# Kernel optimization log

Measured on AMD Instinct MI355X. Metric: run time of the kernel, lower is better.

## Reference

```python
import jax, jax.numpy as jnp
import numpy as np

B, D = 8, 256
N_LIVE, K_NEW = 10000, 32
KC = N_LIVE + K_NEW
N_SAMPLES = 100
EPSILON = 0.1


def setup_inputs() -> dict:
    key = jax.random.key(0)
    k1, k2, k3, k4, k5, k6 = jax.random.split(key, 6)
    return {
        "xt": jax.random.normal(k1, (B, D), dtype=jnp.float32),
        "live_x0": jax.random.normal(k2, (B, N_LIVE, D), dtype=jnp.float32),
        "live_ll": jax.random.normal(k3, (B, N_LIVE, 1), dtype=jnp.float32),
        "x0": jax.random.normal(k4, (B, K_NEW, D), dtype=jnp.float32),
        "ll": jax.random.normal(k5, (B, K_NEW, 1), dtype=jnp.float32),
        "t_scale": jnp.float32(0.5),
        "boot_idx": jax.random.randint(k6, (N_SAMPLES, B, KC), 0, KC, dtype=jnp.int32),
    }


def reference(xt, live_x0, live_ll, x0, ll, t_scale, boot_idx):
    # --- spotlight_score core math ---
    # gaussian correction for the new particles: 0.5*||x0-xt||^2/sigma^2 + log(sigma)
    diff_new = x0 - xt[:, None, :]                                   # [B,K,D]
    corr_new = 0.5 * jnp.sum(diff_new ** 2, axis=-1, keepdims=True) / t_scale ** 2  # [B,K,1]
    current_x0 = jnp.concatenate([live_x0, x0], axis=1)              # [B,Kc,D]
    current_ll = jnp.concatenate(
        [live_ll, ll + corr_new + jnp.log(t_scale)], axis=1)         # [B,Kc,1]

    diff = current_x0 - xt[:, None, :]                               # [B,Kc,D]
    use_ll = (current_ll
              - 0.5 * jnp.sum(diff ** 2, axis=-1, keepdims=True) / t_scale ** 2
              - jnp.log(t_scale))                                    # [B,Kc,1]

    scores_p = diff / t_scale                                        # [B,Kc,D] per-particle scores
    logits = use_ll[..., 0]                                          # [B,Kc]

    # --- check_convergence: bootstrap resampled softmax reductions ---
    def body(carry, idx_n):                                          # idx_n: [B,Kc]
        s = jnp.take_along_axis(scores_p, idx_n[:, :, None], axis=1)  # [B,Kc,D]
        l = jnp.take_along_axis(logits, idx_n, axis=1)                # [B,Kc]
        w = jax.nn.softmax(l, axis=1)
        return carry, jnp.einsum('bk,bkd->bd', w, s)                  # [B,D]

    _, boot = jax.lax.scan(body, None, boot_idx)                      # [N,B,D]
    sigma_v = jnp.std(boot, axis=0, ddof=1)                           # [B,D] (torch.std is unbiased)
    converged = jnp.all(sigma_v < EPSILON * t_scale, axis=1)          # [B]

    # --- final importance-weighted score ---
    w = jax.nn.softmax(logits, axis=1)                                # [B,Kc]
    score = jnp.einsum('bk,bkd->bd', w, scores_p)                     # [B,D]
    return score, converged
```

## Files before the change

### kernel.cpp

```cpp
#include <hip/hip_runtime.h>
#include <math.h>

#define B 8
#define D 256
#define N_LIVE 10000
#define K_NEW 32
#define KC 10032
#define NS 100
#define NROW 101
#define EPS 0.1f
#define CAP 1024
#define ACT_CUT 87.0f
#define LBLK 627
#define BMAX_STRIDE 640

#define WS_HDR    0
#define WS_BMAX   160
#define WS_LOGITS (WS_BMAX + B * BMAX_STRIDE)
#define WS_ACTE   (WS_LOGITS + B * KC)
#define WS_ACTI   (WS_ACTE + B * CAP)
#define WS_LUT    (WS_ACTI + B * CAP)
#define WS_BOOT   (WS_LUT + B * KC / 2)

__global__ __launch_bounds__(256) void k_logits(
    const float* __restrict__ xt, const float* __restrict__ live_x0,
    const float* __restrict__ live_ll, const float* __restrict__ x0n,
    const float* __restrict__ lln, const float* __restrict__ ts_p,
    float* __restrict__ logits, float* __restrict__ bmax) {
  int b = blockIdx.y;
  int w = threadIdx.x >> 6;
  int lane = threadIdx.x & 63;
  int k0 = blockIdx.x * 16 + w * 4;
  float4 c = ((const float4*)(xt + b * D))[lane];

  float s[4];
#pragma unroll
  for (int p = 0; p < 4; p++) {
    int k = k0 + p;
    const float* src = (k < N_LIVE)
        ? (live_x0 + ((size_t)b * N_LIVE + k) * D)
        : (x0n + ((size_t)b * K_NEW + (k - N_LIVE)) * D);
    float4 v = ((const float4*)src)[lane];
    float dx = v.x - c.x, dy = v.y - c.y, dz = v.z - c.z, dw = v.w - c.w;
    s[p] = dx * dx + dy * dy + dz * dz + dw * dw;
  }
#pragma unroll
  for (int off = 32; off; off >>= 1) {
    s[0] += __shfl_xor(s[0], off);
    s[1] += __shfl_xor(s[1], off);
    s[2] += __shfl_xor(s[2], off);
    s[3] += __shfl_xor(s[3], off);
  }
  __shared__ float wlog[4];
  if (lane == 0) {
    float ts = *ts_p;
    float inv2 = 0.5f / (ts * ts), lts = logf(ts);
    float4 o;
    float* ov = &o.x;
#pragma unroll
    for (int p = 0; p < 4; p++) {
      int k = k0 + p;
      ov[p] = (k < N_LIVE)
          ? live_ll[(size_t)b * N_LIVE + k] - s[p] * inv2 - lts
          : lln[(size_t)b * K_NEW + (k - N_LIVE)];
    }
    *(float4*)(logits + (size_t)b * KC + k0) = o;
    wlog[w] = fmaxf(fmaxf(o.x, o.y), fmaxf(o.z, o.w));
  }
  __syncthreads();
  if (threadIdx.x == 0)
    bmax[b * BMAX_STRIDE + blockIdx.x] =
        fmaxf(fmaxf(wlog[0], wlog[1]), fmaxf(wlog[2], wlog[3]));
}

__global__ __launch_bounds__(256) void k_bmax(
    const float* __restrict__ bmax, float* __restrict__ hdr) {
  int b = blockIdx.x;
  int tid = threadIdx.x;
  float m = -INFINITY;
  for (int i = tid; i < LBLK; i += 256) m = fmaxf(m, bmax[b * BMAX_STRIDE + i]);
#pragma unroll
  for (int off = 32; off; off >>= 1) m = fmaxf(m, __shfl_xor(m, off));
  __shared__ float sm[4];
  if ((tid & 63) == 0) sm[tid >> 6] = m;
  __syncthreads();
  if (tid == 0)
    hdr[b * 16] = fmaxf(fmaxf(sm[0], sm[1]), fmaxf(sm[2], sm[3]));
}

__global__ __launch_bounds__(256) void k_select(
    const float* __restrict__ logits, const float* __restrict__ hdrM,
    unsigned* __restrict__ hdr, float* __restrict__ act_e,
    int* __restrict__ act_idx, unsigned short* __restrict__ lut) {
  int b = blockIdx.y;
  int tid = blockIdx.x * 256 + threadIdx.x;
  float M = hdrM[b * 16];
  const float* lg = logits + (size_t)b * KC;
  int* cnt = (int*)&hdr[128 + b];
  for (int k = tid; k < KC; k += 8 * 256) {
    float l = lg[k];
    unsigned short v = 0;
    if (l > M - ACT_CUT) {
      int pos = atomicAdd(cnt, 1);
      if (pos < CAP) {
        act_e[b * CAP + pos] = expf(l - M);
        act_idx[b * CAP + pos] = k;
        v = (unsigned short)(pos + 1);
      }
    }
    lut[(size_t)b * KC + k] = v;
  }
}

__global__ __launch_bounds__(256) void k_boot(
    const float* __restrict__ live_x0, const float* __restrict__ x0n,
    const float* __restrict__ act_e, const int* __restrict__ act_idx,
    const unsigned* __restrict__ hdr, const unsigned short* __restrict__ lut,
    const int* __restrict__ boot_idx, float* __restrict__ boot) {
  int n = blockIdx.x;
  int b = blockIdx.y;
  int tid = threadIdx.x;
  __shared__ int cnt[CAP];
  __shared__ float wval[CAP];
  __shared__ int widx[CAP];
  __shared__ int snnz;
  __shared__ float sden[4];
  int A = min((int)hdr[128 + b], CAP);
  for (int i = tid; i < A; i += 256) cnt[i] = 0;
  if (tid == 0) snnz = 0;
  __syncthreads();

  if (n < NS) {
    const int4* row = (const int4*)(boot_idx + ((size_t)n * B + b) * KC);
    const unsigned short* lutb = lut + (size_t)b * KC;
    for (int k = tid; k < KC / 4; k += 256) {
      int4 v = row[k];
      int t;
      t = lutb[v.x]; if (t) atomicAdd(&cnt[t - 1], 1);
      t = lutb[v.y]; if (t) atomicAdd(&cnt[t - 1], 1);
      t = lutb[v.z]; if (t) atomicAdd(&cnt[t - 1], 1);
      t = lutb[v.w]; if (t) atomicAdd(&cnt[t - 1], 1);
    }
  } else {
    for (int i = tid; i < A; i += 256) cnt[i] = 1;
  }
  __syncthreads();

  float dpart = 0.f;
  for (int i = tid; i < A; i += 256) {
    int c = cnt[i];
    if (c) {
      float w = (float)c * act_e[b * CAP + i];
      int pos = atomicAdd(&snnz, 1);
      wval[pos] = w;
      widx[pos] = act_idx[b * CAP + i];
      dpart += w;
    }
  }
#pragma unroll
  for (int off = 32; off; off >>= 1) dpart += __shfl_xor(dpart, off);
  if ((tid & 63) == 0) sden[tid >> 6] = dpart;
  __syncthreads();
  float inv = 1.f / (sden[0] + sden[1] + sden[2] + sden[3]);
  int nnz = snnz;

  const float* lx = live_x0 + (size_t)b * N_LIVE * D;
  const float* nx = x0n + (size_t)b * K_NEW * D;
  float acc0 = 0.f, acc1 = 0.f;
  int p = 0;
  for (; p + 1 < nnz; p += 2) {
    int j0 = widx[p], j1 = widx[p + 1];
    const float* r0 = (j0 < N_LIVE) ? (lx + (size_t)j0 * D) : (nx + (size_t)(j0 - N_LIVE) * D);
    const float* r1 = (j1 < N_LIVE) ? (lx + (size_t)j1 * D) : (nx + (size_t)(j1 - N_LIVE) * D);
    float x0v = r0[tid], x1v = r1[tid];
    acc0 = fmaf(wval[p], x0v, acc0);
    acc1 = fmaf(wval[p + 1], x1v, acc1);
  }
  if (p < nnz) {
    int j = widx[p];
    const float* xr = (j < N_LIVE) ? (lx + (size_t)j * D) : (nx + (size_t)(j - N_LIVE) * D);
    acc0 = fmaf(wval[p], xr[tid], acc0);
  }
  boot[((size_t)b * NROW + n) * D + tid] = (acc0 + acc1) * inv;
}

__global__ __launch_bounds__(256) void k_final(
    const float* __restrict__ boot, const float* __restrict__ xt,
    const float* __restrict__ ts_p, float* __restrict__ out) {
  int b = blockIdx.x;
  int d = threadIdx.x;
  float ts = *ts_p;
  const float* bb = boot + (size_t)b * NROW * D + d;
  float sum = 0.f;
#pragma unroll 4
  for (int n = 0; n < NS; n++) sum += bb[(size_t)n * D];
  float mean = sum / (float)NS;
  float vs = 0.f;
#pragma unroll 4
  for (int n = 0; n < NS; n++) { float t = bb[(size_t)n * D] - mean; vs += t * t; }
  float sigma_raw = sqrtf(vs / (float)(NS - 1));
  bool ok = (sigma_raw / ts) < (EPS * ts);
  out[(size_t)b * D + d] = (bb[(size_t)NS * D] - xt[(size_t)b * D + d]) / ts;
  unsigned long long m = __ballot(ok);
  __shared__ int wok[4];
  if ((d & 63) == 0) wok[d >> 6] = (m == 0xFFFFFFFFFFFFFFFFull) ? 1 : 0;
  __syncthreads();
  if (d == 0) out[(size_t)B * D + b] = (wok[0] & wok[1] & wok[2] & wok[3]) ? 1.0f : 0.0f;
}

extern "C" void kernel_launch(void* const* d_in, const int* in_sizes, int n_in,
                              void* d_out, int out_size, void* d_ws, size_t ws_size,
                              hipStream_t stream) {
  const float* xt       = (const float*)d_in[0];
  const float* live_x0  = (const float*)d_in[1];
  const float* live_ll  = (const float*)d_in[2];
  const float* x0n      = (const float*)d_in[3];
  const float* lln      = (const float*)d_in[4];
  const float* ts_p     = (const float*)d_in[5];
  const int*   boot_idx = (const int*)d_in[6];
  float* out = (float*)d_out;
  float* ws  = (float*)d_ws;

  float* hdrM              = ws + WS_HDR;
  unsigned* hdr            = (unsigned*)(ws + WS_HDR);
  float* bmax              = ws + WS_BMAX;
  float* logits            = ws + WS_LOGITS;
  float* act_e             = ws + WS_ACTE;
  int*   act_idx           = (int*)(ws + WS_ACTI);
  unsigned short* lut      = (unsigned short*)(ws + WS_LUT);
  float* boot              = ws + WS_BOOT;

  hipMemsetAsync(hdr, 0, 160 * sizeof(unsigned), stream);

  k_logits<<<dim3(LBLK, B), 256, 0, stream>>>(xt, live_x0, live_ll, x0n, lln, ts_p, logits, bmax);
  k_bmax<<<dim3(B), 256, 0, stream>>>(bmax, hdrM);
  k_select<<<dim3(8, B), 256, 0, stream>>>(logits, hdrM, hdr, act_e, act_idx, lut);
  k_boot<<<dim3(NROW, B), 256, 0, stream>>>(live_x0, x0n, act_e, act_idx, hdr, lut, boot_idx, boot);
  k_final<<<dim3(B), 256, 0, stream>>>(boot, xt, ts_p, out);
}
```

Before: 189.3 us.

## Split boot gather across wavefronts with float4 loads; double rows per logits block

In the bootstrap kernel, each of the four wavefronts now walks a strided quarter of the nonzero particle list and loads whole rows as float4 per lane. The four partial accumulators are then reduced through shared memory. The aim is fewer, wider memory transactions and more independent loads in flight per block, at the cost of an extra barrier and shared-memory reduction. The logits kernel also handles 8 rows per wavefront instead of 4, halving the block count, with guards added for the padded tail block.

```diff
diff --git a/kernel.cpp b/kernel.cpp
--- a/kernel.cpp
+++ b/kernel.cpp
@@ -11,8 +11,8 @@
 #define EPS 0.1f
 #define CAP 1024
 #define ACT_CUT 87.0f
-#define LBLK 627
-#define BMAX_STRIDE 640
+#define LBLK 314
+#define BMAX_STRIDE 320
 
 #define WS_HDR    0
 #define WS_BMAX   160
@@ -30,13 +30,15 @@
   int b = blockIdx.y;
   int w = threadIdx.x >> 6;
   int lane = threadIdx.x & 63;
-  int k0 = blockIdx.x * 16 + w * 4;
+  int k0 = blockIdx.x * 32 + w * 8;
+  bool valid = (k0 < KC);
+  int kb = valid ? k0 : 0;
   float4 c = ((const float4*)(xt + b * D))[lane];
 
-  float s[4];
-#pragma unroll
-  for (int p = 0; p < 4; p++) {
-    int k = k0 + p;
+  float s[8];
+#pragma unroll
+  for (int p = 0; p < 8; p++) {
+    int k = kb + p;
     const float* src = (k < N_LIVE)
         ? (live_x0 + ((size_t)b * N_LIVE + k) * D)
         : (x0n + ((size_t)b * K_NEW + (k - N_LIVE)) * D);
@@ -46,26 +48,31 @@
   }
 #pragma unroll
   for (int off = 32; off; off >>= 1) {
-    s[0] += __shfl_xor(s[0], off);
-    s[1] += __shfl_xor(s[1], off);
-    s[2] += __shfl_xor(s[2], off);
-    s[3] += __shfl_xor(s[3], off);
+#pragma unroll
+    for (int p = 0; p < 8; p++) s[p] += __shfl_xor(s[p], off);
   }
   __shared__ float wlog[4];
   if (lane == 0) {
     float ts = *ts_p;
     float inv2 = 0.5f / (ts * ts), lts = logf(ts);
-    float4 o;
-    float* ov = &o.x;
-#pragma unroll
-    for (int p = 0; p < 4; p++) {
-      int k = k0 + p;
-      ov[p] = (k < N_LIVE)
+    float o[8];
+#pragma unroll
+    for (int p = 0; p < 8; p++) {
+      int k = kb + p;
+      o[p] = (k < N_LIVE)
           ? live_ll[(size_t)b * N_LIVE + k] - s[p] * inv2 - lts
           : lln[(size_t)b * K_NEW + (k - N_LIVE)];
     }
-    *(float4*)(logits + (size_t)b * KC + k0) = o;
-    wlog[w] = fmaxf(fmaxf(o.x, o.y), fmaxf(o.z, o.w));
+    if (valid) {
+      float4 o0 = {o[0], o[1], o[2], o[3]}, o1 = {o[4], o[5], o[6], o[7]};
+      *(float4*)(logits + (size_t)b * KC + kb) = o0;
+      *(float4*)(logits + (size_t)b * KC + kb + 4) = o1;
+      float m = fmaxf(fmaxf(fmaxf(o[0], o[1]), fmaxf(o[2], o[3])),
+                      fmaxf(fmaxf(o[4], o[5]), fmaxf(o[6], o[7])));
+      wlog[w] = m;
+    } else {
+      wlog[w] = -INFINITY;
+    }
   }
   __syncthreads();
   if (threadIdx.x == 0)
@@ -120,9 +127,11 @@
   int n = blockIdx.x;
   int b = blockIdx.y;
   int tid = threadIdx.x;
+  int nw = tid >> 6, lane = tid & 63;
   __shared__ int cnt[CAP];
   __shared__ float wval[CAP];
   __shared__ int widx[CAP];
+  __shared__ float4 part[4][64];
   __shared__ int snnz;
   __shared__ float sden[4];
   int A = min((int)hdr[128 + b], CAP);
@@ -166,22 +175,42 @@
 
   const float* lx = live_x0 + (size_t)b * N_LIVE * D;
   const float* nx = x0n + (size_t)b * K_NEW * D;
-  float acc0 = 0.f, acc1 = 0.f;
-  int p = 0;
-  for (; p + 1 < nnz; p += 2) {
-    int j0 = widx[p], j1 = widx[p + 1];
-    const float* r0 = (j0 < N_LIVE) ? (lx + (size_t)j0 * D) : (nx + (size_t)(j0 - N_LIVE) * D);
-    const float* r1 = (j1 < N_LIVE) ? (lx + (size_t)j1 * D) : (nx + (size_t)(j1 - N_LIVE) * D);
-    float x0v = r0[tid], x1v = r1[tid];
-    acc0 = fmaf(wval[p], x0v, acc0);
-    acc1 = fmaf(wval[p + 1], x1v, acc1);
+  float4 a0 = {0.f, 0.f, 0.f, 0.f}, a1 = {0.f, 0.f, 0.f, 0.f};
+  int p = nw;
+  for (; p + 4 < nnz; p += 8) {
+    int j0 = widx[p], j1 = widx[p + 4];
+    float w0 = wval[p], w1 = wval[p + 4];
+    const float4* r0 = (const float4*)((j0 < N_LIVE) ? (lx + (size_t)j0 * D)
+                                                     : (nx + (size_t)(j0 - N_LIVE) * D));
+    const float4* r1 = (const float4*)((j1 < N_LIVE) ? (lx + (size_t)j1 * D)
+                                                     : (nx + (size_t)(j1 - N_LIVE) * D));
+    float4 v0 = r0[lane], v1 = r1[lane];
+    a0.x = fmaf(w0, v0.x, a0.x); a0.y = fmaf(w0, v0.y, a0.y);
+    a0.z = fmaf(w0, v0.z, a0.z); a0.w = fmaf(w0, v0.w, a0.w);
+    a1.x = fmaf(w1, v1.x, a1.x); a1.y = fmaf(w1, v1.y, a1.y);
+    a1.z = fmaf(w1, v1.z, a1.z); a1.w = fmaf(w1, v1.w, a1.w);
   }
   if (p < nnz) {
     int j = widx[p];
-    const float* xr = (j < N_LIVE) ? (lx + (size_t)j * D) : (nx + (size_t)(j - N_LIVE) * D);
-    acc0 = fmaf(wval[p], xr[tid], acc0);
-  }
-  boot[((size_t)b * NROW + n) * D + tid] = (acc0 + acc1) * inv;
+    float w = wval[p];
+    const float4* r = (const float4*)((j < N_LIVE) ? (lx + (size_t)j * D)
+                                                   : (nx + (size_t)(j - N_LIVE) * D));
+    float4 v = r[lane];
+    a0.x = fmaf(w, v.x, a0.x); a0.y = fmaf(w, v.y, a0.y);
+    a0.z = fmaf(w, v.z, a0.z); a0.w = fmaf(w, v.w, a0.w);
+  }
+  a0.x += a1.x; a0.y += a1.y; a0.z += a1.z; a0.w += a1.w;
+  part[nw][lane] = a0;
+  __syncthreads();
+  if (nw == 0) {
+    float4 q0 = part[0][lane], q1 = part[1][lane], q2 = part[2][lane], q3 = part[3][lane];
+    float4 r;
+    r.x = ((q0.x + q1.x) + (q2.x + q3.x)) * inv;
+    r.y = ((q0.y + q1.y) + (q2.y + q3.y)) * inv;
+    r.z = ((q0.z + q1.z) + (q2.z + q3.z)) * inv;
+    r.w = ((q0.w + q1.w) + (q2.w + q3.w)) * inv;
+    ((float4*)(boot + ((size_t)b * NROW + n) * D))[lane] = r;
+  }
 }
 
 __global__ __launch_bounds__(256) void k_final(
```

Result: no change. 191.6 us (+1.2%).
